# Kernel tuning notes

Hardware: AMD Instinct MI355X
Metric: run time of the kernel (lower is better)

## Reference

```python
import jax, jax.numpy as jnp
import numpy as np

EPS = 0.1  # residual scale from __init__


def setup_inputs() -> dict:
    key = jax.random.key(0)
    ks = jax.random.split(key, 13)
    T, B, E = 8, 4096, 16          # terms, batch(queries), predicates(edges)
    F = 1024                        # feature_dim = 2*emb_dim (emb_dim=512)
    M = 2 * F + 2                   # message_dim = 4*emb_dim + 2 = 2050
    H = 4096                        # hidden_dim

    def lin(k, fan_in, shape):
        return jax.random.normal(k, shape, jnp.float32) / np.sqrt(fan_in)

    return {
        "term_emb": jax.random.normal(ks[0], (T, B, F), jnp.float32),
        "pred_emb": jax.random.normal(ks[1], (E, B, F), jnp.float32),
        "W1": lin(ks[2], M, (M, H)),
        "b1": jnp.zeros((H,), jnp.float32),
        "W2": lin(ks[3], H, (H, F)),
        "b2": jnp.zeros((F,), jnp.float32),
        "M1": lin(ks[4], F, (F, H)),
        "mb1": jnp.zeros((H,), jnp.float32),
        "M2": lin(ks[5], H, (H, F)),
        "mb2": jnp.zeros((F,), jnp.float32),
        "head_idx": jax.random.randint(ks[6], (E,), 0, T, jnp.int32),
        "tail_idx": jax.random.randint(ks[7], (E,), 0, T, jnp.int32),
        "sign_bits": jax.random.randint(ks[8], (E,), 0, 2, jnp.int32),
    }


def reference(term_emb, pred_emb, W1, b1, W2, b2, M1, mb1, M2, mb2,
              head_idx, tail_idx, sign_bits):
    # term_emb: [T,B,F], pred_emb: [E,B,F]
    T = term_emb.shape[0]
    E, B, F = pred_emb.shape
    dt = pred_emb.dtype

    sign = (1.0 - 2.0 * sign_bits.astype(dt))[:, None, None]   # [E,1,1], +-1
    ones = jnp.ones((E, B, 1), dt)
    s_ones = sign * ones                                        # [E,B,1]

    h = term_emb[head_idx]                                      # gather [E,B,F]
    t = term_emb[tail_idx]                                      # gather [E,B,F]

    # message to head: [head_emb, pred_emb, +1, sign]
    # message to tail: [tail_emb, pred_emb, -1, sign]
    msg_h = jnp.concatenate([h, pred_emb, ones, s_ones], axis=-1)   # [E,B,M]
    msg_t = jnp.concatenate([t, pred_emb, -ones, s_ones], axis=-1)  # [E,B,M]

    msgs = jnp.concatenate([msg_h, msg_t], axis=0)              # [2E,B,M]
    seg = jnp.concatenate([head_idx, tail_idx], axis=0)         # [2E]
    agg = jax.ops.segment_sum(msgs, seg, num_segments=T)        # [T,B,M]

    # encoder MLP + eps residual
    enc = jax.nn.relu(agg @ W1 + b1) @ W2 + b2                  # [T,B,F]
    x = enc + EPS * term_emb

    # update MLP (layers == 1)
    out = jax.nn.relu(x @ M1 + mb1) @ M2 + mb2                  # [T,B,F]
    return out
```

## Files before the change

### kernel.cpp

```cpp
#include <hip/hip_runtime.h>
#include <hip/hip_bf16.h>
#include <cstdint>

typedef unsigned short u16;
typedef __attribute__((ext_vector_type(8))) u16 u16x8;
typedef __attribute__((ext_vector_type(8))) short s16x8;
typedef __attribute__((ext_vector_type(4))) float f32x4;

#define AS1(p) ((const __attribute__((address_space(1))) void*)(p))
#define AS3(p) ((__attribute__((address_space(3))) void*)(p))

__device__ __forceinline__ u16 f2bf(float f){
  union{float f; uint32_t i;} x; x.f = f;
  uint32_t r = x.i + 0x7fff + ((x.i>>16)&1);
  return (u16)(r>>16);
}

__global__ void transpose_f32_bf16(const float* __restrict__ in, u16* __restrict__ out,
                                   int K, int N){
  __shared__ u16 tile[32][33];
  const int tid = threadIdx.x;
  const int bx = blockIdx.x, by = blockIdx.y;
  const int xl = tid & 31, yl = tid >> 5;
  #pragma unroll
  for (int r = 0; r < 4; ++r){
    int y = by*32 + yl + r*8;
    tile[yl + r*8][xl] = f2bf(in[(size_t)y*N + bx*32 + xl]);
  }
  __syncthreads();
  #pragma unroll
  for (int r = 0; r < 4; ++r){
    int oy = bx*32 + yl + r*8;
    int ox = by*32 + xl;
    out[(size_t)oy*K + ox] = tile[xl][yl + r*8];
  }
}

__global__ void build_bias1(const float* __restrict__ W1, const float* __restrict__ b1,
                            const int* __restrict__ head, const int* __restrict__ tail,
                            const int* __restrict__ sign, float* __restrict__ bias1){
  int idx = blockIdx.x*256 + threadIdx.x;
  int t = idx >> 12, h = idx & 4095;
  float cH = 0.f, cS = 0.f;
  #pragma unroll
  for (int e = 0; e < 16; ++e){
    float s = 1.f - 2.f*(float)sign[e];
    if (head[e] == t){ cH += 1.f; cS += s; }
    if (tail[e] == t){ cH -= 1.f; cS += s; }
  }
  bias1[idx] = b1[h] + cH*W1[(size_t)2048*4096 + h] + cS*W1[(size_t)2049*4096 + h];
}

__global__ void build_x1(const float* __restrict__ term, const float* __restrict__ pred,
                         const int* __restrict__ head, const int* __restrict__ tail,
                         u16* __restrict__ X1, int r0){
  int idx = blockIdx.x*256 + threadIdx.x;
  int lr = idx >> 8;
  int c8 = (idx & 255) * 8;
  int grow = r0 + lr;
  int t = grow >> 12;
  int b = grow & 4095;
  float v[8];
  if (c8 < 1024){
    int deg = 0;
    #pragma unroll
    for (int e = 0; e < 16; ++e) deg += (head[e]==t) + (tail[e]==t);
    float d = (float)deg;
    const float4* p = (const float4*)(term + (size_t)grow*1024 + c8);
    float4 lo = p[0], hi = p[1];
    v[0]=d*lo.x; v[1]=d*lo.y; v[2]=d*lo.z; v[3]=d*lo.w;
    v[4]=d*hi.x; v[5]=d*hi.y; v[6]=d*hi.z; v[7]=d*hi.w;
  } else {
    int f = c8 - 1024;
    #pragma unroll
    for (int j = 0; j < 8; ++j) v[j] = 0.f;
    #pragma unroll
    for (int e = 0; e < 16; ++e){
      int w = (head[e]==t) + (tail[e]==t);
      if (w){
        const float4* p = (const float4*)(pred + ((size_t)e<<22) + ((size_t)b<<10) + f);
        float4 lo = p[0], hi = p[1];
        float fw = (float)w;
        v[0]+=fw*lo.x; v[1]+=fw*lo.y; v[2]+=fw*lo.z; v[3]+=fw*lo.w;
        v[4]+=fw*hi.x; v[5]+=fw*hi.y; v[6]+=fw*hi.z; v[7]+=fw*hi.w;
      }
    }
  }
  u16x8 o;
  #pragma unroll
  for (int j = 0; j < 8; ++j) o[j] = f2bf(v[j]);
  *(u16x8*)(X1 + (size_t)lr*2048 + c8) = o;
}

#define FENCE() asm volatile("" ::: "memory")
#define BAR()   do{ FENCE(); __builtin_amdgcn_s_barrier(); FENCE(); }while(0)
#define VM2()   asm volatile("s_waitcnt vmcnt(2)" ::: "memory")
#define VM4()   asm volatile("s_waitcnt vmcnt(4)" ::: "memory")

#define STAGE(isB, slot, half, kt) do{ \
    const u16* _s = (isB ? bStage : aStage) + ((half) ? halfStride : (size_t)0) + ((size_t)(kt) << 6); \
    u16* _d = &LDS[(isB ? 32768 : 0) + (slot)*16384 + (half)*8192 + tid*8]; \
    __builtin_amdgcn_global_load_lds(AS1(_s), AS3(_d), 16, 0, 0); \
    __builtin_amdgcn_global_load_lds(AS1(_s + q2s), AS3(_d + 4096), 16, 0, 0); \
  }while(0)

#define LOADA(slot, rh) do{ \
    _Pragma("unroll") \
    for (int ii = 0; ii < 4; ++ii){ \
      af[ii][0] = *(const s16x8*)&LDS[(slot)*16384 + aB + ((rh)*4+ii)*1024 + xv0]; \
      af[ii][1] = *(const s16x8*)&LDS[(slot)*16384 + aB + ((rh)*4+ii)*1024 + xv1]; \
    } }while(0)

#define LOADB01(slot) do{ \
    _Pragma("unroll") \
    for (int jj = 0; jj < 2; ++jj){ \
      bfr[jj][0] = *(const s16x8*)&LDS[32768 + (slot)*16384 + bB + jj*1024 + xv0]; \
      bfr[jj][1] = *(const s16x8*)&LDS[32768 + (slot)*16384 + bB + jj*1024 + xv1]; \
    } }while(0)

#define LOADB23(slot) do{ \
    _Pragma("unroll") \
    for (int jj = 2; jj < 4; ++jj){ \
      bfr[jj][0] = *(const s16x8*)&LDS[32768 + (slot)*16384 + bB + jj*1024 + xv0]; \
      bfr[jj][1] = *(const s16x8*)&LDS[32768 + (slot)*16384 + bB + jj*1024 + xv1]; \
    } }while(0)

#define MFMAQ(rh, ch) do{ \
    _Pragma("unroll") \
    for (int hh = 0; hh < 2; ++hh){ \
      _Pragma("unroll") \
      for (int ii = 0; ii < 4; ++ii){ \
        _Pragma("unroll") \
        for (int jj = 0; jj < 2; ++jj){ \
          acc[(rh)*4+ii][(ch)*2+jj] = __builtin_amdgcn_mfma_f32_16x16x32_bf16(af[ii][hh], bfr[(ch)*2+jj][hh], acc[(rh)*4+ii][(ch)*2+jj], 0,0,0); \
        } } } }while(0)

#define PRIO_MFMA(rh, ch) do{ \
    __builtin_amdgcn_s_setprio(1); MFMAQ(rh, ch); __builtin_amdgcn_s_setprio(0); }while(0)

template<int MODE>
__launch_bounds__(512, 2)
__global__ void gemm256(const u16* __restrict__ A, const u16* __restrict__ Bt,
                        void* __restrict__ Cv, int N, int K, int r0,
                        const float* __restrict__ bias_mat,
                        const float* __restrict__ bias_vec,
                        const float* __restrict__ resid){
  __shared__ u16 LDS[65536];
  const int tid = threadIdx.x;
  const int lane = tid & 63;
  const int wid = tid >> 6;
  const int wr = wid >> 2, wc = wid & 3;
  const int frow = lane & 15, fgrp = lane >> 4;

  int nwg = gridDim.x * gridDim.y;
  int orig = blockIdx.y * gridDim.x + blockIdx.x;
  int id = orig;
  if ((nwg & 7) == 0){ int cpx = nwg >> 3; id = (orig & 7) * cpx + (orig >> 3); }
  const int bx = id % gridDim.x, by = id / gridDim.x;
  const int row0 = by * 256, col0 = bx * 256;

  const size_t rowK = (size_t)(tid >> 3) * K;
  const int sg8 = (((tid & 7) ^ ((tid >> 3) & 7)) << 3);
  const u16* aStage = A  + (size_t)row0 * K + rowK + sg8;
  const u16* bStage = Bt + (size_t)col0 * K + rowK + sg8;
  const size_t halfStride = (size_t)128 * K;
  const size_t q2s = (size_t)64 * K;

  const int xv0 = ((fgrp)     ^ (frow & 7)) << 3;
  const int xv1 = ((4 + fgrp) ^ (frow & 7)) << 3;
  const int aB = wr * 8192 + frow * 64;
  const int bB = (wc >> 1) * 8192 + (wc & 1) * 4096 + frow * 64;

  f32x4 acc[8][4];
  #pragma unroll
  for (int i = 0; i < 8; ++i)
    #pragma unroll
    for (int j = 0; j < 4; ++j) acc[i][j] = (f32x4){0.f,0.f,0.f,0.f};
  s16x8 af[4][2], bfr[4][2];

  const int NT = K >> 6;
  const int NI = NT >> 1;

  STAGE(1,0,0,0); STAGE(1,0,1,0); STAGE(0,0,0,0); STAGE(0,0,1,0);
  STAGE(1,1,0,1); STAGE(1,1,1,1);
  VM4(); BAR();

  for (int i = 0; i < NI; ++i){
    const int kt1 = 2*i + 1;
    const int kn0 = (2*i + 2 < NT) ? 2*i + 2 : NT - 2;
    const int kn1 = (2*i + 3 < NT) ? 2*i + 3 : NT - 1;
    LOADA(0,0); LOADB01(0);
    STAGE(0,1,0,kt1);
    BAR();
    PRIO_MFMA(0,0);
    LOADB23(0);
    STAGE(0,1,1,kt1);
    BAR();
    PRIO_MFMA(0,1);
    LOADA(0,1);
    BAR();
    PRIO_MFMA(1,1);
    STAGE(1,0,0,kn0);
    VM2();
    BAR();
    PRIO_MFMA(1,0);
    LOADA(1,0); LOADB01(1);
    STAGE(1,0,1,kn0);
    BAR();
    PRIO_MFMA(0,0);
    LOADB23(1);
    STAGE(0,0,0,kn0);
    BAR();
    PRIO_MFMA(0,1);
    LOADA(1,1);
    STAGE(0,0,1,kn0);
    BAR();
    PRIO_MFMA(1,1);
    STAGE(1,1,0,kn1); STAGE(1,1,1,kn1);
    VM4();
    BAR();
    PRIO_MFMA(1,0);
  }

  #pragma unroll
  for (int i2 = 0; i2 < 8; ++i2){
    #pragma unroll
    for (int j2 = 0; j2 < 4; ++j2){
      #pragma unroll
      for (int r = 0; r < 4; ++r){
        int lrow = row0 + wr*128 + i2*16 + fgrp*4 + r;
        int col  = col0 + wc*64 + j2*16 + frow;
        float v = acc[i2][j2][r];
        if (MODE == 0){
          int grow = r0 + lrow;
          v += bias_mat[(size_t)(grow >> 12)*N + col];
          v = fmaxf(v, 0.f);
          ((u16*)Cv)[(size_t)lrow*N + col] = f2bf(v);
        } else if (MODE == 1){
          int grow = r0 + lrow;
          v += bias_vec[col] + 0.1f*resid[(size_t)grow*1024 + col];
          ((u16*)Cv)[(size_t)lrow*N + col] = f2bf(v);
        } else if (MODE == 2){
          v += bias_vec[col];
          v = fmaxf(v, 0.f);
          ((u16*)Cv)[(size_t)lrow*N + col] = f2bf(v);
        } else {
          v += bias_vec[col];
          ((float*)Cv)[(size_t)lrow*N + col] = v;
        }
      }
    }
  }
}

extern "C" void kernel_launch(void* const* d_in, const int* in_sizes, int n_in,
                              void* d_out, int out_size, void* d_ws, size_t ws_size,
                              hipStream_t stream){
  const float* term = (const float*)d_in[0];
  const float* pred = (const float*)d_in[1];
  const float* W1   = (const float*)d_in[2];
  const float* b1   = (const float*)d_in[3];
  const float* W2   = (const float*)d_in[4];
  const float* b2   = (const float*)d_in[5];
  const float* M1   = (const float*)d_in[6];
  const float* mb1  = (const float*)d_in[7];
  const float* M2   = (const float*)d_in[8];
  const float* mb2  = (const float*)d_in[9];
  const int* head = (const int*)d_in[10];
  const int* tail = (const int*)d_in[11];
  const int* sign = (const int*)d_in[12];
  float* out = (float*)d_out;

  char* ws = (char*)d_ws;
  u16* W1T = (u16*)ws;  ws += (size_t)4096*2048*2;
  u16* W2T = (u16*)ws;  ws += (size_t)1024*4096*2;
  u16* M1T = (u16*)ws;  ws += (size_t)4096*1024*2;
  u16* M2T = (u16*)ws;  ws += (size_t)1024*4096*2;
  float* bias1 = (float*)ws; ws += (size_t)8*4096*4;
  size_t used = (size_t)(ws - (char*)d_ws);

  int R = 32768;
  while (R > 256 && used + (size_t)R*12288 > ws_size) R >>= 1;
  u16* bufA = (u16*)ws;
  u16* bufB = (u16*)(ws + (size_t)R*2048*2);

  transpose_f32_bf16<<<dim3(4096/32, 2048/32), 256, 0, stream>>>(W1, W1T, 2048, 4096);
  transpose_f32_bf16<<<dim3(1024/32, 4096/32), 256, 0, stream>>>(W2, W2T, 4096, 1024);
  transpose_f32_bf16<<<dim3(4096/32, 1024/32), 256, 0, stream>>>(M1, M1T, 1024, 4096);
  transpose_f32_bf16<<<dim3(1024/32, 4096/32), 256, 0, stream>>>(M2, M2T, 4096, 1024);
  build_bias1<<<dim3(8*4096/256), 256, 0, stream>>>(W1, b1, head, tail, sign, bias1);

  for (int r0 = 0; r0 < 32768; r0 += R){
    build_x1<<<dim3(R), 256, 0, stream>>>(term, pred, head, tail, bufA, r0);
    gemm256<0><<<dim3(4096/256, R/256), 512, 0, stream>>>(bufA, W1T, bufB, 4096, 2048, r0, bias1, nullptr, nullptr);
    gemm256<1><<<dim3(1024/256, R/256), 512, 0, stream>>>(bufB, W2T, bufA, 1024, 4096, r0, nullptr, b2, term);
    gemm256<2><<<dim3(4096/256, R/256), 512, 0, stream>>>(bufA, M1T, bufB, 4096, 1024, r0, nullptr, mb1, nullptr);
    gemm256<3><<<dim3(1024/256, R/256), 512, 0, stream>>>(bufB, M2T, out + (size_t)r0*1024, 1024, 4096, r0, nullptr, mb2, nullptr);
  }
}
```

Baseline: 1.349 ms.

## Load GEMM B fragments directly from global memory, stage only A in LDS

The GEMM kernel stops staging the B (weight) tile through LDS. Each wave now loads its B fragments straight from global memory into registers, and only A is double-buffered in LDS, which halves shared memory use. The main loop is rescheduled with fewer barriers, without explicit vmcnt waits or setprio, and without redundant clamped tail loads. The aim is less LDS traffic and less barrier overhead. The cost is exposed global-load latency on B and the loss of tight vmcnt control over when the LDS staging completes, which could be a correctness risk.

```diff
diff --git a/kernel.cpp b/kernel.cpp
--- a/kernel.cpp
+++ b/kernel.cpp
@@ -94,35 +94,24 @@
 
 #define FENCE() asm volatile("" ::: "memory")
 #define BAR()   do{ FENCE(); __builtin_amdgcn_s_barrier(); FENCE(); }while(0)
-#define VM2()   asm volatile("s_waitcnt vmcnt(2)" ::: "memory")
-#define VM4()   asm volatile("s_waitcnt vmcnt(4)" ::: "memory")
-
-#define STAGE(isB, slot, half, kt) do{ \
-    const u16* _s = (isB ? bStage : aStage) + ((half) ? halfStride : (size_t)0) + ((size_t)(kt) << 6); \
-    u16* _d = &LDS[(isB ? 32768 : 0) + (slot)*16384 + (half)*8192 + tid*8]; \
-    __builtin_amdgcn_global_load_lds(AS1(_s), AS3(_d), 16, 0, 0); \
-    __builtin_amdgcn_global_load_lds(AS1(_s + q2s), AS3(_d + 4096), 16, 0, 0); \
-  }while(0)
+
+#define STAGE_Q(slot, q, kt) \
+    __builtin_amdgcn_global_load_lds( \
+        AS1(aStage + (size_t)(q)*64*K + ((size_t)(kt) << 6)), \
+        AS3(&LDS[(slot)*16384 + (q)*4096 + tid*8]), 16, 0, 0)
 
 #define LOADA(slot, rh) do{ \
     _Pragma("unroll") \
     for (int ii = 0; ii < 4; ++ii){ \
-      af[ii][0] = *(const s16x8*)&LDS[(slot)*16384 + aB + ((rh)*4+ii)*1024 + xv0]; \
-      af[ii][1] = *(const s16x8*)&LDS[(slot)*16384 + aB + ((rh)*4+ii)*1024 + xv1]; \
+      af[ii][0] = *(const s16x8*)&LDS[(slot)*16384 + aQ + (rh)*4096 + ii*1024 + xv0]; \
+      af[ii][1] = *(const s16x8*)&LDS[(slot)*16384 + aQ + (rh)*4096 + ii*1024 + xv1]; \
     } }while(0)
 
-#define LOADB01(slot) do{ \
+#define LOADB_G(kt) do{ \
     _Pragma("unroll") \
-    for (int jj = 0; jj < 2; ++jj){ \
-      bfr[jj][0] = *(const s16x8*)&LDS[32768 + (slot)*16384 + bB + jj*1024 + xv0]; \
-      bfr[jj][1] = *(const s16x8*)&LDS[32768 + (slot)*16384 + bB + jj*1024 + xv1]; \
-    } }while(0)
-
-#define LOADB23(slot) do{ \
-    _Pragma("unroll") \
-    for (int jj = 2; jj < 4; ++jj){ \
-      bfr[jj][0] = *(const s16x8*)&LDS[32768 + (slot)*16384 + bB + jj*1024 + xv0]; \
-      bfr[jj][1] = *(const s16x8*)&LDS[32768 + (slot)*16384 + bB + jj*1024 + xv1]; \
+    for (int jj = 0; jj < 4; ++jj){ \
+      bfr[jj][0] = *(const s16x8*)(bRow + (size_t)jj*K16 + ((size_t)(kt) << 6)); \
+      bfr[jj][1] = *(const s16x8*)(bRow + (size_t)jj*K16 + ((size_t)(kt) << 6) + 32); \
     } }while(0)
 
 #define MFMAQ(rh, ch) do{ \
@@ -135,9 +124,6 @@
           acc[(rh)*4+ii][(ch)*2+jj] = __builtin_amdgcn_mfma_f32_16x16x32_bf16(af[ii][hh], bfr[(ch)*2+jj][hh], acc[(rh)*4+ii][(ch)*2+jj], 0,0,0); \
         } } } }while(0)
 
-#define PRIO_MFMA(rh, ch) do{ \
-    __builtin_amdgcn_s_setprio(1); MFMAQ(rh, ch); __builtin_amdgcn_s_setprio(0); }while(0)
-
 template<int MODE>
 __launch_bounds__(512, 2)
 __global__ void gemm256(const u16* __restrict__ A, const u16* __restrict__ Bt,
@@ -145,7 +131,7 @@
                         const float* __restrict__ bias_mat,
                         const float* __restrict__ bias_vec,
                         const float* __restrict__ resid){
-  __shared__ u16 LDS[65536];
+  __shared__ u16 LDS[32768];
   const int tid = threadIdx.x;
   const int lane = tid & 63;
   const int wid = tid >> 6;
@@ -159,17 +145,14 @@
   const int bx = id % gridDim.x, by = id / gridDim.x;
   const int row0 = by * 256, col0 = bx * 256;
 
-  const size_t rowK = (size_t)(tid >> 3) * K;
-  const int sg8 = (((tid & 7) ^ ((tid >> 3) & 7)) << 3);
-  const u16* aStage = A  + (size_t)row0 * K + rowK + sg8;
-  const u16* bStage = Bt + (size_t)col0 * K + rowK + sg8;
-  const size_t halfStride = (size_t)128 * K;
-  const size_t q2s = (size_t)64 * K;
+  const u16* aStage = A + (size_t)row0 * K + (size_t)(tid >> 3) * K
+                        + (((tid & 7) ^ ((tid >> 3) & 7)) << 3);
+  const u16* bRow = Bt + (size_t)(col0 + wc*64 + frow) * K + fgrp*8;
+  const size_t K16 = (size_t)K * 16;
 
   const int xv0 = ((fgrp)     ^ (frow & 7)) << 3;
   const int xv1 = ((4 + fgrp) ^ (frow & 7)) << 3;
-  const int aB = wr * 8192 + frow * 64;
-  const int bB = (wc >> 1) * 8192 + (wc & 1) * 4096 + frow * 64;
+  const int aQ = wr * 8192 + frow * 64;
 
   f32x4 acc[8][4];
   #pragma unroll
@@ -181,45 +164,31 @@
   const int NT = K >> 6;
   const int NI = NT >> 1;
 
-  STAGE(1,0,0,0); STAGE(1,0,1,0); STAGE(0,0,0,0); STAGE(0,0,1,0);
-  STAGE(1,1,0,1); STAGE(1,1,1,1);
-  VM4(); BAR();
+  STAGE_Q(0,0,0); STAGE_Q(0,2,0); STAGE_Q(0,1,0); STAGE_Q(0,3,0);
+  STAGE_Q(1,0,1); STAGE_Q(1,2,1);
+  asm volatile("s_waitcnt vmcnt(2)" ::: "memory");
+  BAR();
 
   for (int i = 0; i < NI; ++i){
-    const int kt1 = 2*i + 1;
-    const int kn0 = (2*i + 2 < NT) ? 2*i + 2 : NT - 2;
-    const int kn1 = (2*i + 3 < NT) ? 2*i + 3 : NT - 1;
-    LOADA(0,0); LOADB01(0);
-    STAGE(0,1,0,kt1);
-    BAR();
-    PRIO_MFMA(0,0);
-    LOADB23(0);
-    STAGE(0,1,1,kt1);
-    BAR();
-    PRIO_MFMA(0,1);
+    const int kt0 = 2*i, kt1 = 2*i + 1;
+    LOADB_G(kt0);
+    STAGE_Q(1,1,kt1); STAGE_Q(1,3,kt1);
+    LOADA(0,0);
+    MFMAQ(0,0); MFMAQ(0,1);
+    BAR();
+    if (kt0 + 2 < NT){ STAGE_Q(0,0,kt0+2); STAGE_Q(0,2,kt0+2); }
     LOADA(0,1);
-    BAR();
-    PRIO_MFMA(1,1);
-    STAGE(1,0,0,kn0);
-    VM2();
-    BAR();
-    PRIO_MFMA(1,0);
-    LOADA(1,0); LOADB01(1);
-    STAGE(1,0,1,kn0);
-    BAR();
-    PRIO_MFMA(0,0);
-    LOADB23(1);
-    STAGE(0,0,0,kn0);
-    BAR();
-    PRIO_MFMA(0,1);
+    MFMAQ(1,0); MFMAQ(1,1);
+    BAR();
+    LOADB_G(kt1);
+    if (kt1 + 1 < NT){ STAGE_Q(0,1,kt1+1); STAGE_Q(0,3,kt1+1); }
+    LOADA(1,0);
+    MFMAQ(0,0); MFMAQ(0,1);
+    BAR();
+    if (kt1 + 2 < NT){ STAGE_Q(1,0,kt1+2); STAGE_Q(1,2,kt1+2); }
     LOADA(1,1);
-    STAGE(0,0,1,kn0);
-    BAR();
-    PRIO_MFMA(1,1);
-    STAGE(1,1,0,kn1); STAGE(1,1,1,kn1);
-    VM4();
-    BAR();
-    PRIO_MFMA(1,0);
+    MFMAQ(1,0); MFMAQ(1,1);
+    BAR();
   }
 
   #pragma unroll
```

Measured after the change: 2.150 ms. 59.4% more time.
